# Optimization experiments

Hardware: AMD Instinct MI355X
Metric: run time of the kernel (lower is better)

Reference implementation:

```python
import jax, jax.numpy as jnp
import numpy as np

B, CH, IMG, P = 16, 3, 384, 16
D, HEADS, DH, MLP, DEPTH = 384, 6, 64, 1536, 6
INNER = HEADS * DH
PD = P * P * 5 * CH          # SPT patch dim = 3840
GRID = IMG // P              # 24
NP = GRID * GRID             # 576 patches
SEQ = NP + 1                 # +cls = 577


def layer_norm(x, g, b, eps=1e-5):
    mu = jnp.mean(x, axis=-1, keepdims=True)
    var = jnp.var(x, axis=-1, keepdims=True)
    return (x - mu) * jax.lax.rsqrt(var + eps) * g + b


def spt_shifts(x):
    # F.pad semantics: (left,right,top,bottom) with negative = crop
    s1 = jnp.pad(x, ((0, 0), (0, 0), (0, 0), (1, 0)))[:, :, :, :-1]  # (1,-1,0,0)
    s2 = jnp.pad(x, ((0, 0), (0, 0), (0, 0), (0, 1)))[:, :, :, 1:]   # (-1,1,0,0)
    s3 = jnp.pad(x, ((0, 0), (0, 0), (1, 0), (0, 0)))[:, :, :-1, :]  # (0,0,1,-1)
    s4 = jnp.pad(x, ((0, 0), (0, 0), (0, 1), (0, 0)))[:, :, 1:, :]   # (0,0,-1,1)
    return jnp.concatenate([x, s1, s2, s3, s4], axis=1)  # [b, 5c, H, W]


def patchify(x):
    # 'b c (h p1) (w p2) -> b (h w) (p1 p2 c)'
    b, c, _, _ = x.shape
    x = x.reshape(b, c, GRID, P, GRID, P)
    x = x.transpose(0, 2, 4, 3, 5, 1)  # b h w p1 p2 c
    return x.reshape(b, GRID * GRID, P * P * c)


def setup_inputs():
    key = jax.random.key(0)
    ks = jax.random.split(key, 16)
    img = jax.random.normal(ks[0], (B, CH, IMG, IMG), jnp.float32)
    spt_g = jnp.ones((PD,), jnp.float32)
    spt_b = jnp.zeros((PD,), jnp.float32)
    spt_w = jax.random.normal(ks[1], (PD, D), jnp.float32) * (1.0 / np.sqrt(PD))
    spt_bias = jnp.zeros((D,), jnp.float32)
    pos = jax.random.normal(ks[2], (1, SEQ, D), jnp.float32) * 0.02
    cls = jax.random.normal(ks[3], (1, 1, D), jnp.float32) * 0.02
    attn_g = jnp.ones((DEPTH, D), jnp.float32)
    attn_b = jnp.zeros((DEPTH, D), jnp.float32)
    temp = jnp.full((DEPTH,), np.log(DH ** -0.5), jnp.float32)
    wqkv = jax.random.normal(ks[4], (DEPTH, D, 3 * INNER), jnp.float32) * 0.02
    wout = jax.random.normal(ks[5], (DEPTH, INNER, D), jnp.float32) * 0.02
    bout = jnp.zeros((DEPTH, D), jnp.float32)
    ff_g = jnp.ones((DEPTH, D), jnp.float32)
    ff_b = jnp.zeros((DEPTH, D), jnp.float32)
    w1 = jax.random.normal(ks[6], (DEPTH, D, MLP), jnp.float32) * 0.02
    b1 = jnp.zeros((DEPTH, MLP), jnp.float32)
    w2 = jax.random.normal(ks[7], (DEPTH, MLP, D), jnp.float32) * 0.02
    b2 = jnp.zeros((DEPTH, D), jnp.float32)
    return {"img": img, "spt_g": spt_g, "spt_b": spt_b, "spt_w": spt_w,
            "spt_bias": spt_bias, "pos": pos, "cls": cls, "attn_g": attn_g,
            "attn_b": attn_b, "temp": temp, "wqkv": wqkv, "wout": wout,
            "bout": bout, "ff_g": ff_g, "ff_b": ff_b, "w1": w1, "b1": b1,
            "w2": w2, "b2": b2}


def vit_forward(img, spt_g, spt_b, spt_w, spt_bias, pos, cls, attn_g, attn_b,
                temp, wqkv, wout, bout, ff_g, ff_b, w1, b1, w2, b2):
    # SPT patch embedding
    x = patchify(spt_shifts(img))                      # [b, NP, PD]
    x = layer_norm(x, spt_g, spt_b) @ spt_w + spt_bias  # [b, NP, D]
    b = x.shape[0]
    cls_tok = jnp.broadcast_to(cls, (b, 1, D))
    x = jnp.concatenate([cls_tok, x], axis=1) + pos[:, :SEQ]

    eye = jnp.eye(SEQ, dtype=bool)
    neg = -jnp.finfo(x.dtype).max

    def block(x, p):
        ag, ab, t, wq, wo, bo, fg, fb, W1, B1, W2, B2 = p
        h = layer_norm(x, ag, ab)
        qkv = h @ wq                                   # [b, n, 3*inner]
        q, k, v = jnp.split(qkv, 3, axis=-1)
        q = q.reshape(b, SEQ, HEADS, DH).transpose(0, 2, 1, 3)
        k = k.reshape(b, SEQ, HEADS, DH).transpose(0, 2, 1, 3)
        v = v.reshape(b, SEQ, HEADS, DH).transpose(0, 2, 1, 3)
        dots = jnp.einsum('bhid,bhjd->bhij', q, k) * jnp.exp(t)
        dots = jnp.where(eye, neg, dots)               # diagonal mask (LSA)
        attn = jax.nn.softmax(dots, axis=-1)
        out = jnp.einsum('bhij,bhjd->bhid', attn, v)
        out = out.transpose(0, 2, 1, 3).reshape(b, SEQ, INNER)
        x = out @ wo + bo + x
        h = layer_norm(x, fg, fb)
        x = jax.nn.gelu(h @ W1 + B1, approximate=False) @ W2 + B2 + x
        return x, None

    params = (attn_g, attn_b, temp, wqkv, wout, bout, ff_g, ff_b, w1, b1, w2, b2)
    x, _ = jax.lax.scan(block, x, params)
    return x


def reference(img, spt_g, spt_b, spt_w, spt_bias, pos, cls, attn_g, attn_b,
              temp, wqkv, wout, bout, ff_g, ff_b, w1, b1, w2, b2):
    return vit_forward(img, spt_g, spt_b, spt_w, spt_bias, pos, cls, attn_g,
                       attn_b, temp, wqkv, wout, bout, ff_g, ff_b, w1, b1,
                       w2, b2)
```

## Files before the change

kernel.cpp:

```cpp
#include <hip/hip_runtime.h>

typedef unsigned short ushort_t;
typedef __bf16 bf16x8 __attribute__((ext_vector_type(8)));
typedef float f32x4 __attribute__((ext_vector_type(4)));

#define SEQ_ 577
#define D_ 384
#define NTOK (16 * 577)

enum { M_QKV = 0, M_OUT, M_MLP1, M_MLP2 };

__device__ inline float b2f(ushort_t u) {
    unsigned int x = ((unsigned int)u) << 16;
    float f; __builtin_memcpy(&f, &x, 4); return f;
}
__device__ inline ushort_t f2b(float f) {
    unsigned int x; __builtin_memcpy(&x, &f, 4);
    x = x + 0x7fffu + ((x >> 16) & 1u);
    return (ushort_t)(x >> 16);
}

__device__ void transpose_tile(const float* __restrict__ src,
                               ushort_t* __restrict__ dst,
                               int ldn, int ldk, int k0, int n0)
{
    __shared__ float t[64][65];
    const int tid = threadIdx.x;
    const int c = tid & 63, rr = tid >> 6;
#pragma unroll
    for (int i = 0; i < 16; i++) {
        int kl = rr + i * 4;
        t[kl][c] = src[(size_t)(k0 + kl) * ldn + n0 + c];
    }
    __syncthreads();
#pragma unroll
    for (int i = 0; i < 16; i++) {
        int nl = rr + i * 4;
        dst[(size_t)(n0 + nl) * ldk + k0 + c] = f2b(t[c][nl]);
    }
}

__global__ __launch_bounds__(256) void prep_spt_kernel(
    const float* __restrict__ w, ushort_t* __restrict__ wt)
{
    transpose_tile(w, wt, 384, 3840, blockIdx.x * 64, blockIdx.y * 64);
}

__global__ __launch_bounds__(256) void prep_all_kernel(
    const float* __restrict__ wqkv, const float* __restrict__ wout,
    const float* __restrict__ w1, const float* __restrict__ w2,
    ushort_t* __restrict__ W6)
{
    int id = blockIdx.x;
    int l = id / 432;
    int r = id - l * 432;
    ushort_t* qkv_t  = W6 + (size_t)l * 1769472;
    ushort_t* wout_t = qkv_t + 442368;
    ushort_t* w1_t   = wout_t + 147456;
    ushort_t* w2_t   = w1_t + 589824;
    const float* wq = wqkv + (size_t)l * 442368;
    const float* wo = wout + (size_t)l * 147456;
    const float* W1 = w1 + (size_t)l * 589824;
    const float* W2 = w2 + (size_t)l * 589824;
    if (r < 108) {
        int kt = r / 18, nt = r % 18;
        transpose_tile(wq, qkv_t, 1152, 384, kt * 64, nt * 64);
    } else if (r < 144) {
        r -= 108; int kt = r / 6, nt = r % 6;
        transpose_tile(wo, wout_t, 384, 384, kt * 64, nt * 64);
    } else if (r < 288) {
        r -= 144; int kt = r / 24, nt = r % 24;
        transpose_tile(W1, w1_t, 1536, 384, kt * 64, nt * 64);
    } else {
        r -= 288; int kt = r / 6, nt = r % 6;
        transpose_tile(W2, w2_t, 384, 1536, kt * 64, nt * 64);
    }
}

template <int MODE>
__global__ __launch_bounds__(256) void gemm12864(
    const ushort_t* __restrict__ A, const ushort_t* __restrict__ Bt,
    ushort_t* __restrict__ Co, const float* __restrict__ bias,
    int M, int K, int ldc)
{
    __shared__ __align__(16) ushort_t As[2][128][40];
    __shared__ __align__(16) ushort_t Bs[2][64][40];

    const int gx = gridDim.x;
    const int nwg = gx * gridDim.y;
    const int f = blockIdx.y * gx + blockIdx.x;
    const int q = nwg >> 3, rr_ = nwg & 7;
    const int xcd = f & 7, ii = f >> 3;
    const int swz = (xcd < rr_ ? xcd * (q + 1) : rr_ * (q + 1) + (xcd - rr_) * q) + ii;
    const int bx = swz % gx, by = swz / gx;

    const int tid = threadIdx.x;
    const int rowBase = by * 128;
    const int colBase = bx * 64;
    const int nk = K >> 5;
    const int lr = tid >> 2, lk = (tid & 3) * 8;
    const int wv = tid >> 6, lane = tid & 63;
    const int wm = (wv >> 1) * 64, wn = (wv & 1) * 32;
    const int m16 = lane & 15, q4 = lane >> 4, kb = q4 * 8;

    const ushort_t* pa0 = A + (size_t)(rowBase + lr) * K + lk;
    const ushort_t* pa1 = pa0 + (size_t)64 * K;
    const ushort_t* pb  = Bt + (size_t)(colBase + lr) * K + lk;

    f32x4 acc[4][2];
#pragma unroll
    for (int i = 0; i < 4; i++)
#pragma unroll
        for (int j = 0; j < 2; j++) acc[i][j] = (f32x4){0.f, 0.f, 0.f, 0.f};

    uint4 Ua0, Ua1, Ub, Va0, Va1, Vb;
    auto gloadU = [&](int kt) {
        Ua0 = *(const uint4*)(pa0 + kt * 32);
        Ua1 = *(const uint4*)(pa1 + kt * 32);
        Ub  = *(const uint4*)(pb + kt * 32);
    };
    auto gloadV = [&](int kt) {
        Va0 = *(const uint4*)(pa0 + kt * 32);
        Va1 = *(const uint4*)(pa1 + kt * 32);
        Vb  = *(const uint4*)(pb + kt * 32);
    };
    auto swriteU = [&](int buf) {
        *(uint4*)&As[buf][lr][lk] = Ua0;
        *(uint4*)&As[buf][64 + lr][lk] = Ua1;
        *(uint4*)&Bs[buf][lr][lk] = Ub;
    };
    auto swriteV = [&](int buf) {
        *(uint4*)&As[buf][lr][lk] = Va0;
        *(uint4*)&As[buf][64 + lr][lk] = Va1;
        *(uint4*)&Bs[buf][lr][lk] = Vb;
    };
    auto compute = [&](int buf) {
        bf16x8 af[4];
#pragma unroll
        for (int mt = 0; mt < 4; mt++)
            af[mt] = *(const bf16x8*)&As[buf][wm + mt * 16 + m16][kb];
        bf16x8 b0 = *(const bf16x8*)&Bs[buf][wn + m16][kb];
        bf16x8 b1 = *(const bf16x8*)&Bs[buf][wn + 16 + m16][kb];
#pragma unroll
        for (int mt = 0; mt < 4; mt++) {
            acc[mt][0] = __builtin_amdgcn_mfma_f32_16x16x32_bf16(af[mt], b0, acc[mt][0], 0, 0, 0);
            acc[mt][1] = __builtin_amdgcn_mfma_f32_16x16x32_bf16(af[mt], b1, acc[mt][1], 0, 0, 0);
        }
    };

    gloadU(0);
    swriteU(0);
    gloadU(1);
    gloadV(2);
    __syncthreads();

    for (int kt = 0; kt < nk; kt += 2) {
        swriteU(1);
        if (kt + 3 < nk) gloadU(kt + 3);
        compute(0);
        __syncthreads();
        if (kt + 2 < nk) {
            swriteV(0);
            if (kt + 4 < nk) gloadV(kt + 4);
        }
        compute(1);
        __syncthreads();
    }

#pragma unroll
    for (int mt = 0; mt < 4; mt++)
#pragma unroll
        for (int nt = 0; nt < 2; nt++) {
            int col = colBase + wn + nt * 16 + m16;
#pragma unroll
            for (int r = 0; r < 4; r++) {
                int row = rowBase + wm + mt * 16 + q4 * 4 + r;
                if (row >= M) continue;
                float v = acc[mt][nt][r];
                if (MODE == M_QKV) {
                    Co[(size_t)row * ldc + col] = f2b(v);
                } else if (MODE == M_MLP1) {
                    float t = v + bias[col];
                    float u = t * (0.7978845608f + 0.0356774081f * t * t);
                    float e = __builtin_amdgcn_exp2f(2.885390082f * u);
                    float gl = t - t * __builtin_amdgcn_rcpf(e + 1.0f);
                    Co[(size_t)row * ldc + col] = f2b(gl);
                }
            }
        }
}

template <int MODE>
__global__ __launch_bounds__(256) void gemm64(
    const ushort_t* __restrict__ A, const ushort_t* __restrict__ Bt,
    ushort_t* __restrict__ Co, float* __restrict__ resid,
    const float* __restrict__ bias,
    int M, int K, int ldc)
{
    __shared__ __align__(16) ushort_t As[2][64][40];
    __shared__ __align__(16) ushort_t Bs[2][64][40];

    const int gx = gridDim.x;
    const int nwg = gx * gridDim.y;
    const int f = blockIdx.y * gx + blockIdx.x;
    const int q = nwg >> 3, rr_ = nwg & 7;
    const int xcd = f & 7, ii = f >> 3;
    const int swz = (xcd < rr_ ? xcd * (q + 1) : rr_ * (q + 1) + (xcd - rr_) * q) + ii;
    const int bx = swz % gx, by = swz / gx;

    const int tid = threadIdx.x;
    const int rowBase = by * 64;
    const int colBase = bx * 64;
    const int nk = K >> 5;
    const int lr = tid >> 2, lk = (tid & 3) * 8;
    const int wv = tid >> 6, lane = tid & 63;
    const int wm = (wv >> 1) * 32, wn = (wv & 1) * 32;
    const int m16 = lane & 15, q4 = lane >> 4, kb = q4 * 8;

    const ushort_t* pa = A + (size_t)(rowBase + lr) * K + lk;
    const ushort_t* pb = Bt + (size_t)(colBase + lr) * K + lk;

    f32x4 acc[2][2];
#pragma unroll
    for (int i = 0; i < 2; i++)
#pragma unroll
        for (int j = 0; j < 2; j++) acc[i][j] = (f32x4){0.f, 0.f, 0.f, 0.f};

    uint4 Ua, Ub, Va, Vb;
    auto gloadU = [&](int kt) {
        Ua = *(const uint4*)(pa + kt * 32);
        Ub = *(const uint4*)(pb + kt * 32);
    };
    auto gloadV = [&](int kt) {
        Va = *(const uint4*)(pa + kt * 32);
        Vb = *(const uint4*)(pb + kt * 32);
    };
    auto swriteU = [&](int buf) {
        *(uint4*)&As[buf][lr][lk] = Ua;
        *(uint4*)&Bs[buf][lr][lk] = Ub;
    };
    auto swriteV = [&](int buf) {
        *(uint4*)&As[buf][lr][lk] = Va;
        *(uint4*)&Bs[buf][lr][lk] = Vb;
    };
    auto compute = [&](int buf) {
        bf16x8 a0 = *(const bf16x8*)&As[buf][wm + m16][kb];
        bf16x8 a1 = *(const bf16x8*)&As[buf][wm + 16 + m16][kb];
        bf16x8 b0 = *(const bf16x8*)&Bs[buf][wn + m16][kb];
        bf16x8 b1 = *(const bf16x8*)&Bs[buf][wn + 16 + m16][kb];
        acc[0][0] = __builtin_amdgcn_mfma_f32_16x16x32_bf16(a0, b0, acc[0][0], 0, 0, 0);
        acc[0][1] = __builtin_amdgcn_mfma_f32_16x16x32_bf16(a0, b1, acc[0][1], 0, 0, 0);
        acc[1][0] = __builtin_amdgcn_mfma_f32_16x16x32_bf16(a1, b0, acc[1][0], 0, 0, 0);
        acc[1][1] = __builtin_amdgcn_mfma_f32_16x16x32_bf16(a1, b1, acc[1][1], 0, 0, 0);
    };

    gloadU(0);
    swriteU(0);
    gloadU(1);
    gloadV(2);
    __syncthreads();

    for (int kt = 0; kt < nk; kt += 2) {
        swriteU(1);
        if (kt + 3 < nk) gloadU(kt + 3);
        compute(0);
        __syncthreads();
        if (kt + 2 < nk) {
            swriteV(0);
            if (kt + 4 < nk) gloadV(kt + 4);
        }
        compute(1);
        __syncthreads();
    }

#pragma unroll
    for (int im = 0; im < 2; im++)
#pragma unroll
        for (int in = 0; in < 2; in++) {
            int col = colBase + wn + in * 16 + m16;
#pragma unroll
            for (int r = 0; r < 4; r++) {
                int row = rowBase + wm + im * 16 + q4 * 4 + r;
                if (row >= M) continue;
                size_t o = (size_t)row * ldc + col;
                resid[o] = resid[o] + acc[im][in][r] + bias[col];
            }
        }
}

__global__ __launch_bounds__(256) void gemm64_spt_split(
    const ushort_t* __restrict__ A, const ushort_t* __restrict__ Bt,
    float* __restrict__ resid, int rowOff)
{
    __shared__ __align__(16) ushort_t As[2][64][40];
    __shared__ __align__(16) ushort_t Bs[2][64][40];

    const int f = blockIdx.z * 288 + blockIdx.y * 6 + blockIdx.x;
    const int swz = (f & 7) * 144 + (f >> 3);
    const int bz = swz / 288;
    const int rem = swz - bz * 288;
    const int by = rem / 6, bx = rem - by * 6;

    const int K = 3840, nk = 30;
    const int rowBase = by * 64;
    const int colBase = bx * 64;
    const int kbase = bz * 960;

    const int tid = threadIdx.x;
    const int lr = tid >> 2, lk = (tid & 3) * 8;
    const int wv = tid >> 6, lane = tid & 63;
    const int wm = (wv >> 1) * 32, wn = (wv & 1) * 32;
    const int m16 = lane & 15, q4 = lane >> 4, kb = q4 * 8;

    const ushort_t* pa = A + (size_t)(rowBase + lr) * K + kbase + lk;
    const ushort_t* pb = Bt + (size_t)(colBase + lr) * K + kbase + lk;

    f32x4 acc[2][2];
#pragma unroll
    for (int i = 0; i < 2; i++)
#pragma unroll
        for (int j = 0; j < 2; j++) acc[i][j] = (f32x4){0.f, 0.f, 0.f, 0.f};

    uint4 Ua, Ub, Va, Vb;
    auto gloadU = [&](int kt) {
        Ua = *(const uint4*)(pa + kt * 32);
        Ub = *(const uint4*)(pb + kt * 32);
    };
    auto gloadV = [&](int kt) {
        Va = *(const uint4*)(pa + kt * 32);
        Vb = *(const uint4*)(pb + kt * 32);
    };
    auto swriteU = [&](int buf) {
        *(uint4*)&As[buf][lr][lk] = Ua;
        *(uint4*)&Bs[buf][lr][lk] = Ub;
    };
    auto swriteV = [&](int buf) {
        *(uint4*)&As[buf][lr][lk] = Va;
        *(uint4*)&Bs[buf][lr][lk] = Vb;
    };
    auto compute = [&](int buf) {
        bf16x8 a0 = *(const bf16x8*)&As[buf][wm + m16][kb];
        bf16x8 a1 = *(const bf16x8*)&As[buf][wm + 16 + m16][kb];
        bf16x8 b0 = *(const bf16x8*)&Bs[buf][wn + m16][kb];
        bf16x8 b1 = *(const bf16x8*)&Bs[buf][wn + 16 + m16][kb];
        acc[0][0] = __builtin_amdgcn_mfma_f32_16x16x32_bf16(a0, b0, acc[0][0], 0, 0, 0);
        acc[0][1] = __builtin_amdgcn_mfma_f32_16x16x32_bf16(a0, b1, acc[0][1], 0, 0, 0);
        acc[1][0] = __builtin_amdgcn_mfma_f32_16x16x32_bf16(a1, b0, acc[1][0], 0, 0, 0);
        acc[1][1] = __builtin_amdgcn_mfma_f32_16x16x32_bf16(a1, b1, acc[1][1], 0, 0, 0);
    };

    gloadU(0);
    swriteU(0);
    gloadU(1);
    gloadV(2);
    __syncthreads();

    for (int kt = 0; kt < nk; kt += 2) {
        swriteU(1);
        if (kt + 3 < nk) gloadU(kt + 3);
        compute(0);
        __syncthreads();
        if (kt + 2 < nk) {
            swriteV(0);
            if (kt + 4 < nk) gloadV(kt + 4);
        }
        compute(1);
        __syncthreads();
    }

#pragma unroll
    for (int im = 0; im < 2; im++)
#pragma unroll
        for (int in = 0; in < 2; in++) {
            int col = colBase + wn + in * 16 + m16;
#pragma unroll
            for (int r = 0; r < 4; r++) {
                int row = rowBase + wm + im * 16 + q4 * 4 + r;
                int grow = rowOff + row;
                int bb = grow / 576, p = grow - bb * 576;
                size_t o = ((size_t)(bb * SEQ_ + 1 + p)) * D_ + col;
                atomicAdd(&resid[o], acc[im][in][r]);
            }
        }
}

__global__ __launch_bounds__(256) void attn_kernel(
    const ushort_t* __restrict__ qkv, ushort_t* __restrict__ attn,
    const float* __restrict__ temp, int layer)
{
    const int qt = blockIdx.x;
    const int bh = blockIdx.y;
    const int b = bh / 6, hd = bh - b * 6;
    const int tid = threadIdx.x;
    const int wv = tid >> 6, lane = tid & 63;
    const int m16 = lane & 15, q4 = lane >> 4;
    const float sc2 = expf(temp[layer]) * 1.44269504f;

    __shared__ __align__(16) ushort_t Ks[64][72];
    __shared__ __align__(16) ushort_t Vt[64][72];
    __shared__ __align__(16) ushort_t Pw[4][16][72];

    const int qrow = qt * 64 + wv * 16 + m16;
    const int qtok = qrow < SEQ_ ? qrow : SEQ_ - 1;
    const ushort_t* qb = qkv + ((size_t)(b * SEQ_ + qtok)) * 1152 + hd * 64;
    bf16x8 qf0 = *(const bf16x8*)(qb + q4 * 8);
    bf16x8 qf1 = *(const bf16x8*)(qb + 32 + q4 * 8);

    f32x4 accO[4];
#pragma unroll
    for (int dt = 0; dt < 4; dt++) accO[dt] = (f32x4){0.f, 0.f, 0.f, 0.f};
    float l_r[4] = {0.f, 0.f, 0.f, 0.f};

    const int skey = tid >> 2;
    const int scol = (tid & 3) * 16;
    const int vp   = tid & 31;
    const int vdh  = (tid >> 5) * 8;

    for (int kt = 0; kt < 10; kt++) {
        int key = kt * 64 + skey;
        int gkey = key < SEQ_ ? key : 0;
        const ushort_t* kb_ = qkv + ((size_t)(b * SEQ_ + gkey)) * 1152 + 384 + hd * 64;
        uint4 kv0 = *(const uint4*)(kb_ + scol);
        uint4 kv1 = *(const uint4*)(kb_ + scol + 8);
        if (key >= SEQ_) { kv0 = (uint4){0, 0, 0, 0}; kv1 = kv0; }
        int vk0 = kt * 64 + 2 * vp;
        int t0 = vk0 < SEQ_ ? vk0 : 0;
        int t1 = vk0 + 1 < SEQ_ ? vk0 + 1 : 0;
        uint4 va = *(const uint4*)(qkv + ((size_t)(b * SEQ_ + t0)) * 1152 + 768 + hd * 64 + vdh);
        uint4 vb2 = *(const uint4*)(qkv + ((size_t)(b * SEQ_ + t1)) * 1152 + 768 + hd * 64 + vdh);
        if (vk0 >= SEQ_) va = (uint4){0, 0, 0, 0};
        if (vk0 + 1 >= SEQ_) vb2 = (uint4){0, 0, 0, 0};
        __syncthreads();
        *(uint4*)&Ks[skey][scol] = kv0;
        *(uint4*)&Ks[skey][scol + 8] = kv1;
        {
            const ushort_t* e0 = (const ushort_t*)&va;
            const ushort_t* e1 = (const ushort_t*)&vb2;
#pragma unroll
            for (int j = 0; j < 8; j++) {
                unsigned int pack = (unsigned int)e0[j] | ((unsigned int)e1[j] << 16);
                *(unsigned int*)&Vt[vdh + j][2 * vp] = pack;
            }
        }
        __syncthreads();

        f32x4 s[4];
#pragma unroll
        for (int ct = 0; ct < 4; ct++) {
            bf16x8 b0 = *(const bf16x8*)&Ks[ct * 16 + m16][q4 * 8];
            bf16x8 b1 = *(const bf16x8*)&Ks[ct * 16 + m16][32 + q4 * 8];
            f32x4 z = (f32x4){0.f, 0.f, 0.f, 0.f};
            z = __builtin_amdgcn_mfma_f32_16x16x32_bf16(qf0, b0, z, 0, 0, 0);
            z = __builtin_amdgcn_mfma_f32_16x16x32_bf16(qf1, b1, z, 0, 0, 0);
            s[ct] = z;
        }
        const int rowb = qt * 64 + wv * 16 + q4 * 4;
#pragma unroll
        for (int r = 0; r < 4; r++) {
            float rs = 0.f;
#pragma unroll
            for (int ct = 0; ct < 4; ct++) {
                int col = kt * 64 + ct * 16 + m16;
                float v = s[ct][r] * sc2;
                if (col >= SEQ_ || col == rowb + r) v = -1.0e30f;
                float p = __builtin_amdgcn_exp2f(v);
                s[ct][r] = p;
                rs += p;
            }
            rs += __shfl_xor(rs, 1);
            rs += __shfl_xor(rs, 2);
            rs += __shfl_xor(rs, 4);
            rs += __shfl_xor(rs, 8);
            l_r[r] += rs;
        }
#pragma unroll
        for (int ct = 0; ct < 4; ct++)
#pragma unroll
            for (int r = 0; r < 4; r++)
                Pw[wv][q4 * 4 + r][ct * 16 + m16] = f2b(s[ct][r]);
        bf16x8 pf0 = *(const bf16x8*)&Pw[wv][m16][q4 * 8];
        bf16x8 pf1 = *(const bf16x8*)&Pw[wv][m16][32 + q4 * 8];
#pragma unroll
        for (int dt = 0; dt < 4; dt++) {
            bf16x8 vb0 = *(const bf16x8*)&Vt[dt * 16 + m16][q4 * 8];
            bf16x8 vb1 = *(const bf16x8*)&Vt[dt * 16 + m16][32 + q4 * 8];
            f32x4 o = accO[dt];
            o = __builtin_amdgcn_mfma_f32_16x16x32_bf16(pf0, vb0, o, 0, 0, 0);
            o = __builtin_amdgcn_mfma_f32_16x16x32_bf16(pf1, vb1, o, 0, 0, 0);
            accO[dt] = o;
        }
    }

    const int rowb = qt * 64 + wv * 16 + q4 * 4;
#pragma unroll
    for (int r = 0; r < 4; r++) {
        int grow = rowb + r;
        if (grow >= SEQ_) continue;
        float inv = 1.f / l_r[r];
        ushort_t* op = attn + ((size_t)(b * SEQ_ + grow)) * 384 + hd * 64;
#pragma unroll
        for (int dt = 0; dt < 4; dt++)
            op[dt * 16 + m16] = f2b(accO[dt][r] * inv);
    }
}

__global__ __launch_bounds__(256) void spt_ln_kernel(
    const float* __restrict__ img, const float* __restrict__ gg,
    const float* __restrict__ bb_, ushort_t* __restrict__ Xn, int r0)
{
    int bp = r0 + blockIdx.x;
    int b = bp / 576, p = bp - b * 576;
    int ph = p / 24, pw = p - ph * 24;

    __shared__ float vals[3840];
    __shared__ float red[10];

    const int tid = threadIdx.x;
    const int p1 = tid >> 4, p2 = tid & 15;

    float s = 0.f, sq = 0.f;
#pragma unroll
    for (int plane = 0; plane < 15; plane++) {
        int g5 = plane / 3, ch = plane - g5 * 3;
        int row = ph * 16 + p1, col = pw * 16 + p2;
        if (g5 == 1) col -= 1;
        else if (g5 == 2) col += 1;
        else if (g5 == 3) row -= 1;
        else if (g5 == 4) row += 1;
        float v = 0.f;
        if (row >= 0 && row < 384 && col >= 0 && col < 384)
            v = img[((size_t)(b * 3 + ch) * 384 + row) * 384 + col];
        vals[tid * 15 + plane] = v;
        s += v; sq += v * v;
    }
#pragma unroll
    for (int off = 32; off > 0; off >>= 1) {
        s += __shfl_xor(s, off);
        sq += __shfl_xor(sq, off);
    }
    int wid = tid >> 6;
    if ((tid & 63) == 0) { red[wid] = s; red[4 + wid] = sq; }
    __syncthreads();
    if (tid == 0) {
        float S = red[0] + red[1] + red[2] + red[3];
        float Q = red[4] + red[5] + red[6] + red[7];
        float mean = S / 3840.f;
        float var = Q / 3840.f - mean * mean;
        red[8] = mean;
        red[9] = rsqrtf(var + 1e-5f);
    }
    __syncthreads();
    float mean = red[8], rstd = red[9];
#pragma unroll
    for (int i = 0; i < 15; i++) {
        int k = tid + i * 256;
        float v = (vals[k] - mean) * rstd * gg[k] + bb_[k];
        Xn[(size_t)blockIdx.x * 3840 + k] = f2b(v);
    }
}

__global__ __launch_bounds__(256) void ln_kernel(
    const float* __restrict__ x, const float* __restrict__ g,
    const float* __restrict__ b, ushort_t* __restrict__ h)
{
    int row = blockIdx.x * 4 + (threadIdx.x >> 6);
    int lane = threadIdx.x & 63;
    const float4* xr = (const float4*)(x + (size_t)row * 384);
    float4 a = xr[lane];
    float4 c = (lane < 32) ? xr[64 + lane] : make_float4(0.f, 0.f, 0.f, 0.f);
    float s = a.x + a.y + a.z + a.w + c.x + c.y + c.z + c.w;
    float sq = a.x * a.x + a.y * a.y + a.z * a.z + a.w * a.w
             + c.x * c.x + c.y * c.y + c.z * c.z + c.w * c.w;
#pragma unroll
    for (int off = 32; off > 0; off >>= 1) {
        s += __shfl_xor(s, off);
        sq += __shfl_xor(sq, off);
    }
    float mean = s / 384.f;
    float var = sq / 384.f - mean * mean;
    float rstd = rsqrtf(var + 1e-5f);
    const float4* g4 = (const float4*)g;
    const float4* b4 = (const float4*)b;
    ushort_t* hr = h + (size_t)row * 384;
    {
        float4 gv = g4[lane], bv = b4[lane];
        unsigned int lo = (unsigned int)f2b((a.x - mean) * rstd * gv.x + bv.x)
                        | ((unsigned int)f2b((a.y - mean) * rstd * gv.y + bv.y) << 16);
        unsigned int hi = (unsigned int)f2b((a.z - mean) * rstd * gv.z + bv.z)
                        | ((unsigned int)f2b((a.w - mean) * rstd * gv.w + bv.w) << 16);
        *(uint2*)&hr[lane * 4] = make_uint2(lo, hi);
    }
    if (lane < 32) {
        float4 gv = g4[64 + lane], bv = b4[64 + lane];
        unsigned int lo = (unsigned int)f2b((c.x - mean) * rstd * gv.x + bv.x)
                        | ((unsigned int)f2b((c.y - mean) * rstd * gv.y + bv.y) << 16);
        unsigned int hi = (unsigned int)f2b((c.z - mean) * rstd * gv.z + bv.z)
                        | ((unsigned int)f2b((c.w - mean) * rstd * gv.w + bv.w) << 16);
        *(uint2*)&hr[256 + lane * 4] = make_uint2(lo, hi);
    }
}

__global__ void init_x_kernel(const float* __restrict__ cls,
                              const float* __restrict__ pos,
                              const float* __restrict__ spt_bias,
                              float* __restrict__ x)
{
    int s = blockIdx.x, b = blockIdx.y, d = threadIdx.x;
    float base = (s == 0) ? cls[d] : spt_bias[d];
    x[((size_t)b * SEQ_ + s) * D_ + d] = base + pos[(size_t)s * D_ + d];
}

extern "C" void kernel_launch(void* const* d_in, const int* in_sizes, int n_in,
                              void* d_out, int out_size, void* d_ws, size_t ws_size,
                              hipStream_t stream)
{
    const float* img      = (const float*)d_in[0];
    const float* spt_g    = (const float*)d_in[1];
    const float* spt_b    = (const float*)d_in[2];
    const float* spt_w    = (const float*)d_in[3];
    const float* spt_bias = (const float*)d_in[4];
    const float* pos      = (const float*)d_in[5];
    const float* clsp     = (const float*)d_in[6];
    const float* attn_g   = (const float*)d_in[7];
    const float* attn_b   = (const float*)d_in[8];
    const float* temp     = (const float*)d_in[9];
    const float* wqkv     = (const float*)d_in[10];
    const float* wout     = (const float*)d_in[11];
    const float* bout     = (const float*)d_in[12];
    const float* ff_g     = (const float*)d_in[13];
    const float* ff_b     = (const float*)d_in[14];
    const float* w1       = (const float*)d_in[15];
    const float* b1       = (const float*)d_in[16];
    const float* w2       = (const float*)d_in[17];
    const float* b2       = (const float*)d_in[18];

    float* x = (float*)d_out;

    char* base = (char*)d_ws;
    ushort_t* qkv   = (ushort_t*)base;
    ushort_t* attn  = (ushort_t*)(base + (size_t)NTOK * 1152 * 2);
    ushort_t* Xn    = (ushort_t*)base;
    ushort_t* gbuf  = (ushort_t*)base;
    ushort_t* spt_wt = (ushort_t*)(base + 23592960);
    char* p2 = base + (size_t)NTOK * 1536 * 2;
    ushort_t* h  = (ushort_t*)p2;
    char* p3 = p2 + (size_t)NTOK * 384 * 2;
    ushort_t* W6 = (ushort_t*)p3;

    prep_all_kernel<<<2592, 256, 0, stream>>>(wqkv, wout, w1, w2, W6);
    prep_spt_kernel<<<dim3(60, 6), 256, 0, stream>>>(spt_w, spt_wt);
    init_x_kernel<<<dim3(SEQ_, 16), 384, 0, stream>>>(clsp, pos, spt_bias, x);

    for (int c = 0; c < 3; c++) {
        int r0 = c * 3072;
        spt_ln_kernel<<<3072, 256, 0, stream>>>(img, spt_g, spt_b, Xn, r0);
        gemm64_spt_split<<<dim3(6, 48, 4), 256, 0, stream>>>(Xn, spt_wt, x, r0);
    }

    for (int l = 0; l < 6; l++) {
        ushort_t* qkv_t  = W6 + (size_t)l * 1769472;
        ushort_t* wout_t = qkv_t + 442368;
        ushort_t* w1_t   = wout_t + 147456;
        ushort_t* w2_t   = w1_t + 589824;
        ln_kernel<<<NTOK / 4, 256, 0, stream>>>(x, attn_g + l * 384, attn_b + l * 384, h);
        gemm12864<M_QKV><<<dim3(18, 73), 256, 0, stream>>>(
            h, qkv_t, qkv, nullptr, NTOK, 384, 1152);
        attn_kernel<<<dim3(10, 96), 256, 0, stream>>>(qkv, attn, temp, l);
        gemm64<M_OUT><<<dim3(6, 145), 256, 0, stream>>>(
            attn, wout_t, nullptr, x, bout + l * 384, NTOK, 384, 384);
        ln_kernel<<<NTOK / 4, 256, 0, stream>>>(x, ff_g + l * 384, ff_b + l * 384, h);
        gemm12864<M_MLP1><<<dim3(24, 73), 256, 0, stream>>>(
            h, w1_t, gbuf, b1 + l * 1536, NTOK, 384, 1536);
        gemm64<M_MLP2><<<dim3(6, 145), 256, 0, stream>>>(
            gbuf, w2_t, nullptr, x, b2 + l * 384, NTOK, 1536, 384);
    }
}
```

Baseline: 1.188 ms.

## Split-K MLP2 GEMM with atomics, prefetch attention K/V, merge prep kernels

The MLP2 GEMM (K=1536) is split into two K halves across a z grid dimension. Partial results are accumulated into the fp32 residual with atomicAdd, and only the first split adds the bias. This doubles the workgroup count to improve occupancy, at the cost of atomic traffic and nondeterministic summation order. The attention kernel now issues global loads of the next K/V tile before computing on the current one, and the SPT weight transpose is folded into the main prep kernel launch.

```diff
diff --git a/kernel.cpp b/kernel.cpp
--- a/kernel.cpp
+++ b/kernel.cpp
@@ -40,18 +40,19 @@
     }
 }
 
-__global__ __launch_bounds__(256) void prep_spt_kernel(
-    const float* __restrict__ w, ushort_t* __restrict__ wt)
-{
-    transpose_tile(w, wt, 384, 3840, blockIdx.x * 64, blockIdx.y * 64);
-}
-
 __global__ __launch_bounds__(256) void prep_all_kernel(
     const float* __restrict__ wqkv, const float* __restrict__ wout,
     const float* __restrict__ w1, const float* __restrict__ w2,
-    ushort_t* __restrict__ W6)
+    const float* __restrict__ spt_w,
+    ushort_t* __restrict__ W6, ushort_t* __restrict__ spt_wt)
 {
     int id = blockIdx.x;
+    if (id >= 2592) {
+        int r2 = id - 2592;
+        int kt = r2 % 60, nt = r2 / 60;
+        transpose_tile(spt_w, spt_wt, 384, 3840, kt * 64, nt * 64);
+        return;
+    }
     int l = id / 432;
     int r = id - l * 432;
     ushort_t* qkv_t  = W6 + (size_t)l * 1769472;
@@ -190,35 +191,37 @@
         }
 }
 
-template <int MODE>
+template <int MODE, int SPLITZ>
 __global__ __launch_bounds__(256) void gemm64(
     const ushort_t* __restrict__ A, const ushort_t* __restrict__ Bt,
-    ushort_t* __restrict__ Co, float* __restrict__ resid,
-    const float* __restrict__ bias,
+    float* __restrict__ resid, const float* __restrict__ bias,
     int M, int K, int ldc)
 {
     __shared__ __align__(16) ushort_t As[2][64][40];
     __shared__ __align__(16) ushort_t Bs[2][64][40];
 
-    const int gx = gridDim.x;
-    const int nwg = gx * gridDim.y;
-    const int f = blockIdx.y * gx + blockIdx.x;
+    const int gx = gridDim.x, gy = gridDim.y;
+    const int nwg = gx * gy * SPLITZ;
+    const int f = (blockIdx.z * gy + blockIdx.y) * gx + blockIdx.x;
     const int q = nwg >> 3, rr_ = nwg & 7;
     const int xcd = f & 7, ii = f >> 3;
     const int swz = (xcd < rr_ ? xcd * (q + 1) : rr_ * (q + 1) + (xcd - rr_) * q) + ii;
-    const int bx = swz % gx, by = swz / gx;
+    const int bx = swz % gx;
+    const int tmp = swz / gx;
+    const int by = tmp % gy, bz = tmp / gy;
 
     const int tid = threadIdx.x;
     const int rowBase = by * 64;
     const int colBase = bx * 64;
-    const int nk = K >> 5;
+    const int nk = (K >> 5) / SPLITZ;
+    const int kbase = bz * nk * 32;
     const int lr = tid >> 2, lk = (tid & 3) * 8;
     const int wv = tid >> 6, lane = tid & 63;
     const int wm = (wv >> 1) * 32, wn = (wv & 1) * 32;
     const int m16 = lane & 15, q4 = lane >> 4, kb = q4 * 8;
 
-    const ushort_t* pa = A + (size_t)(rowBase + lr) * K + lk;
-    const ushort_t* pb = Bt + (size_t)(colBase + lr) * K + lk;
+    const ushort_t* pa = A + (size_t)(rowBase + lr) * K + kbase + lk;
+    const ushort_t* pb = Bt + (size_t)(colBase + lr) * K + kbase + lk;
 
     f32x4 acc[2][2];
 #pragma unroll
@@ -283,7 +286,12 @@
                 int row = rowBase + wm + im * 16 + q4 * 4 + r;
                 if (row >= M) continue;
                 size_t o = (size_t)row * ldc + col;
-                resid[o] = resid[o] + acc[im][in][r] + bias[col];
+                if (SPLITZ > 1) {
+                    float v = acc[im][in][r] + (bz == 0 ? bias[col] : 0.f);
+                    atomicAdd(&resid[o], v);
+                } else {
+                    resid[o] = resid[o] + acc[im][in][r] + bias[col];
+                }
             }
         }
 }
@@ -416,20 +424,26 @@
     const int vp   = tid & 31;
     const int vdh  = (tid >> 5) * 8;
 
-    for (int kt = 0; kt < 10; kt++) {
+    uint4 kv0, kv1, va, vb2;
+    auto loadKV = [&](int kt) {
         int key = kt * 64 + skey;
         int gkey = key < SEQ_ ? key : 0;
         const ushort_t* kb_ = qkv + ((size_t)(b * SEQ_ + gkey)) * 1152 + 384 + hd * 64;
-        uint4 kv0 = *(const uint4*)(kb_ + scol);
-        uint4 kv1 = *(const uint4*)(kb_ + scol + 8);
+        kv0 = *(const uint4*)(kb_ + scol);
+        kv1 = *(const uint4*)(kb_ + scol + 8);
         if (key >= SEQ_) { kv0 = (uint4){0, 0, 0, 0}; kv1 = kv0; }
         int vk0 = kt * 64 + 2 * vp;
         int t0 = vk0 < SEQ_ ? vk0 : 0;
         int t1 = vk0 + 1 < SEQ_ ? vk0 + 1 : 0;
-        uint4 va = *(const uint4*)(qkv + ((size_t)(b * SEQ_ + t0)) * 1152 + 768 + hd * 64 + vdh);
-        uint4 vb2 = *(const uint4*)(qkv + ((size_t)(b * SEQ_ + t1)) * 1152 + 768 + hd * 64 + vdh);
+        va  = *(const uint4*)(qkv + ((size_t)(b * SEQ_ + t0)) * 1152 + 768 + hd * 64 + vdh);
+        vb2 = *(const uint4*)(qkv + ((size_t)(b * SEQ_ + t1)) * 1152 + 768 + hd * 64 + vdh);
         if (vk0 >= SEQ_) va = (uint4){0, 0, 0, 0};
         if (vk0 + 1 >= SEQ_) vb2 = (uint4){0, 0, 0, 0};
+    };
+
+    loadKV(0);
+
+    for (int kt = 0; kt < 10; kt++) {
         __syncthreads();
         *(uint4*)&Ks[skey][scol] = kv0;
         *(uint4*)&Ks[skey][scol + 8] = kv1;
@@ -443,6 +457,7 @@
             }
         }
         __syncthreads();
+        if (kt + 1 < 10) loadKV(kt + 1);
 
         f32x4 s[4];
 #pragma unroll
@@ -647,8 +662,7 @@
     char* p3 = p2 + (size_t)NTOK * 384 * 2;
     ushort_t* W6 = (ushort_t*)p3;
 
-    prep_all_kernel<<<2592, 256, 0, stream>>>(wqkv, wout, w1, w2, W6);
-    prep_spt_kernel<<<dim3(60, 6), 256, 0, stream>>>(spt_w, spt_wt);
+    prep_all_kernel<<<2952, 256, 0, stream>>>(wqkv, wout, w1, w2, spt_w, W6, spt_wt);
     init_x_kernel<<<dim3(SEQ_, 16), 384, 0, stream>>>(clsp, pos, spt_bias, x);
 
     for (int c = 0; c < 3; c++) {
@@ -666,12 +680,12 @@
         gemm12864<M_QKV><<<dim3(18, 73), 256, 0, stream>>>(
             h, qkv_t, qkv, nullptr, NTOK, 384, 1152);
         attn_kernel<<<dim3(10, 96), 256, 0, stream>>>(qkv, attn, temp, l);
-        gemm64<M_OUT><<<dim3(6, 145), 256, 0, stream>>>(
-            attn, wout_t, nullptr, x, bout + l * 384, NTOK, 384, 384);
+        gemm64<M_OUT, 1><<<dim3(6, 145), 256, 0, stream>>>(
+            attn, wout_t, x, bout + l * 384, NTOK, 384, 384);
         ln_kernel<<<NTOK / 4, 256, 0, stream>>>(x, ff_g + l * 384, ff_b + l * 384, h);
         gemm12864<M_MLP1><<<dim3(24, 73), 256, 0, stream>>>(
             h, w1_t, gbuf, b1 + l * 1536, NTOK, 384, 1536);
-        gemm64<M_MLP2><<<dim3(6, 145), 256, 0, stream>>>(
-            gbuf, w2_t, nullptr, x, b2 + l * 384, NTOK, 1536, 384);
-    }
-}
+        gemm64<M_MLP2, 2><<<dim3(6, 145, 2), 256, 0, stream>>>(
+            gbuf, w2_t, x, b2 + l * 384, NTOK, 1536, 384);
+    }
+}
```

After: 1.246 ms. 4.9% more time.
